# Optimization experiments

Measured on AMD Instinct MI355X. Metric: run time of the kernel, lower is better.

Reference implementation:

```python
import jax, jax.numpy as jnp
import numpy as np

BLUR_SIGMA = 5.0      # init kwarg blur_sigma
N_SIGMAS_PER_SIDE = 4 # fixed in module source
FLOW_AMP = 1.0        # init kwarg flow_amp
N_DIMS = 2            # len(img_shape) - 1


def _gaussian_kernel_2d(sigma, n_sigmas_per_side):
    # separable 2D gaussian spanning n_sigmas_per_side sigmas on each side, sum-normalized
    r = int(round(n_sigmas_per_side * sigma))
    x = np.arange(-r, r + 1, dtype=np.float32)
    g = np.exp(-(x ** 2) / (2.0 * sigma ** 2))
    k = np.outer(g, g)
    k /= k.sum()
    return jnp.asarray(k, dtype=jnp.float32)  # [kh, kw] = [41, 41] for sigma=5


def setup_inputs() -> dict:
    key = jax.random.key(0)
    k1, k2 = jax.random.split(key)
    inputs = jax.random.normal(k1, (16, 512, 512, 1), dtype=jnp.float32)
    # uniform in [0,1); scaled to [-flow_amp, flow_amp) inside reference
    rand_noise = jax.random.uniform(k2, (16, 512, 512, 2), dtype=jnp.float32)
    return {"inputs": inputs, "rand_noise": rand_noise}


def reference(inputs, rand_noise):
    # kernel tiled identically over the n_dims flow channels (depthwise, multiplier=1)
    k2d = _gaussian_kernel_2d(BLUR_SIGMA, N_SIGMAS_PER_SIDE)
    kernel = jnp.tile(k2d[:, :, None, None], (1, 1, 1, N_DIMS))  # HWIO: [41,41,1,2]
    # K.random_uniform(minval=-flow_amp, maxval=flow_amp)
    flow = rand_noise * (2.0 * FLOW_AMP) - FLOW_AMP  # [B,H,W,2]
    # tf.nn.depthwise_conv2d(..., strides=1, padding='SAME')
    out = jax.lax.conv_general_dilated(
        flow, kernel,
        window_strides=(1, 1),
        padding="SAME",
        dimension_numbers=("NHWC", "HWIO", "NHWC"),
        feature_group_count=N_DIMS,
    )  # [B,H,W,2] == reshape to (-1,)+flow_shape (no-op here)
    return out
```

## Files before the change

kernel.cpp:

```cpp
#include <hip/hip_runtime.h>

#define NB   16
#define H    512
#define W    512
#define KW   41
#define HALO 20

#define TX   88
#define TY   32
#define IN_W 128
#define PVV  16
#define PX   11
#define MSTR 129
#define OSTR 89
#define SMEM_F2 (TY * MSTR)

constexpr float G[KW] = {
  0.0003354626f, 0.0007318024f, 0.0015338104f, 0.0030887172f,
  0.0059760229f, 0.0111089965f, 0.0198410947f, 0.0340474548f,
  0.0561347628f, 0.0889216176f, 0.1353352832f, 0.1978986990f,
  0.2780373005f, 0.3753110988f, 0.4867522560f, 0.6065306597f,
  0.7261490371f, 0.8352702114f, 0.9231163464f, 0.9801986733f,
  1.0f,
  0.9801986733f, 0.9231163464f, 0.8352702114f, 0.7261490371f,
  0.6065306597f, 0.4867522560f, 0.3753110988f, 0.2780373005f,
  0.1978986990f, 0.1353352832f, 0.0889216176f, 0.0561347628f,
  0.0340474548f, 0.0198410947f, 0.0111089965f, 0.0059760229f,
  0.0030887172f, 0.0015338104f, 0.0007318024f, 0.0003354626f
};

constexpr float gsum() { float s = 0.f; for (int i = 0; i < KW; ++i) s += G[i]; return s; }
constexpr float INV_S2 = 1.0f / (gsum() * gsum());

__global__ __launch_bounds__(256, 4)
void randflow_blur_kernel(const float* __restrict__ noise, float* __restrict__ out) {
    __shared__ float2 smem[SMEM_F2];

    const int tid = threadIdx.x;
    const int bx  = blockIdx.x;
    const int tx0 = bx * TX;
    const int ty0 = blockIdx.y * TY;
    const int b   = blockIdx.z;
    const float* __restrict__ src = noise + (size_t)b * (H * W * 2);

    {
        const int sx  = tid & 127;
        const int yg  = tid >> 7;
        const int gx  = tx0 + sx - HALO;
        const int cgx = min(max(gx, 0), W - 1);
        const float sa = (gx == cgx) ? 2.0f : 0.0f;
        const float sb = (gx == cgx) ? -1.0f : 0.0f;
        const int  ysb = ty0 + yg * PVV - HALO;
        const float* __restrict__ colp = src + 2 * cgx;

        float2 acc[PVV];
        #pragma unroll
        for (int p = 0; p < PVV; ++p) acc[p] = make_float2(0.f, 0.f);

        #pragma unroll
        for (int j = 0; j < PVV + KW - 1; ++j) {
            const int ys = ysb + j;
            const int cy = min(max(ys, 0), H - 1);
            const float a  = (ys == cy) ? sa : 0.0f;
            const float bb = (ys == cy) ? sb : 0.0f;
            const float2 u = *(const float2*)(colp + (size_t)cy * (W * 2));
            float2 v;
            v.x = __builtin_fmaf(u.x, a, bb);
            v.y = __builtin_fmaf(u.y, a, bb);
            #pragma unroll
            for (int p = 0; p < PVV; ++p) {
                const int t = j - p;
                if (t >= 0 && t < KW) {
                    acc[p].x = __builtin_fmaf(G[t], v.x, acc[p].x);
                    acc[p].y = __builtin_fmaf(G[t], v.y, acc[p].y);
                }
            }
        }
        #pragma unroll
        for (int p = 0; p < PVV; ++p)
            smem[(yg * PVV + p) * MSTR + sx] = acc[p];
    }
    __syncthreads();

    const int y  = tid & 31;
    const int xg = tid >> 5;
    const int x0 = xg * PX;
    float2 facc[PX];
    {
        #pragma unroll
        for (int p = 0; p < PX; ++p) facc[p] = make_float2(0.f, 0.f);
        #pragma unroll
        for (int j = 0; j < PX + KW - 1; ++j) {
            const float2 v = smem[y * MSTR + x0 + j];
            #pragma unroll
            for (int p = 0; p < PX; ++p) {
                const int t = j - p;
                if (t >= 0 && t < KW) {
                    facc[p].x = __builtin_fmaf(G[t], v.x, facc[p].x);
                    facc[p].y = __builtin_fmaf(G[t], v.y, facc[p].y);
                }
            }
        }
    }
    __syncthreads();

    #pragma unroll
    for (int p = 0; p < PX; ++p) {
        float2 r;
        r.x = facc[p].x * INV_S2;
        r.y = facc[p].y * INV_S2;
        smem[y * OSTR + x0 + p] = r;
    }
    __syncthreads();

    #pragma unroll
    for (int p = 0; p < PX; ++p) {
        const int flat = p * 256 + tid;
        const int ry = flat / TX;
        const int rx = flat - ry * TX;
        const int xo = tx0 + rx;
        if (xo < W) {
            const int yo = ty0 + ry;
            *(float2*)(out + (((size_t)b * H + yo) * W + xo) * 2) = smem[ry * OSTR + rx];
        }
    }
}

extern "C" void kernel_launch(void* const* d_in, const int* in_sizes, int n_in,
                              void* d_out, int out_size, void* d_ws, size_t ws_size,
                              hipStream_t stream) {
    const float* noise = (const float*)d_in[1];
    float* out = (float*)d_out;

    dim3 grid((W + TX - 1) / TX, H / TY, NB);
    dim3 block(256);
    randflow_blur_kernel<<<grid, block, 0, stream>>>(noise, out);
}
```

Baseline: 124.6 us.

## Split fused blur into separate vertical and horizontal pass kernels via workspace

```diff
diff --git a/kernel.cpp b/kernel.cpp
--- a/kernel.cpp
+++ b/kernel.cpp
@@ -5,15 +5,6 @@
 #define W    512
 #define KW   41
 #define HALO 20
-
-#define TX   88
-#define TY   32
-#define IN_W 128
-#define PVV  16
-#define PX   11
-#define MSTR 129
-#define OSTR 89
-#define SMEM_F2 (TY * MSTR)
 
 constexpr float G[KW] = {
   0.0003354626f, 0.0007318024f, 0.0015338104f, 0.0030887172f,
@@ -31,6 +22,134 @@
 
 constexpr float gsum() { float s = 0.f; for (int i = 0; i < KW; ++i) s += G[i]; return s; }
 constexpr float INV_S2 = 1.0f / (gsum() * gsum());
+
+#define V_PV   16
+#define V_ROWS (V_PV + KW - 1)
+
+__global__ __launch_bounds__(256, 8)
+void vpass_kernel(const float* __restrict__ noise, float* __restrict__ mid) {
+    const int tid = threadIdx.x;
+
+    int id = blockIdx.x + 2 * (blockIdx.y + 32 * blockIdx.z);
+    id = ((id & 7) << 7) | (id >> 3);
+    const int lx = id & 1;
+    const int ly = (id >> 1) & 31;
+    const int lb = id >> 6;
+
+    const int x  = lx * 256 + tid;
+    const int y0 = ly * V_PV;
+
+    const float* __restrict__ src = noise + ((size_t)lb * H * W + x) * 2;
+    float*       __restrict__ dst = mid   + (((size_t)lb * H + y0) * W + x) * 2;
+
+    float2 acc[V_PV];
+    #pragma unroll
+    for (int p = 0; p < V_PV; ++p) acc[p] = make_float2(0.f, 0.f);
+
+    const int ysb = y0 - HALO;
+    #pragma unroll
+    for (int j = 0; j < V_ROWS; ++j) {
+        const int ys = ysb + j;
+        const int cy = min(max(ys, 0), H - 1);
+        const float a  = (ys == cy) ? 2.0f : 0.0f;
+        const float bb = (ys == cy) ? -1.0f : 0.0f;
+        const float2 u = *(const float2*)(src + (size_t)cy * (W * 2));
+        float2 v;
+        v.x = __builtin_fmaf(u.x, a, bb);
+        v.y = __builtin_fmaf(u.y, a, bb);
+        #pragma unroll
+        for (int p = 0; p < V_PV; ++p) {
+            const int t = j - p;
+            if (t >= 0 && t < KW) {
+                acc[p].x = __builtin_fmaf(G[t], v.x, acc[p].x);
+                acc[p].y = __builtin_fmaf(G[t], v.y, acc[p].y);
+            }
+        }
+    }
+    #pragma unroll
+    for (int p = 0; p < V_PV; ++p)
+        *(float2*)(dst + (size_t)p * (W * 2)) = acc[p];
+}
+
+#define HX   256
+#define HR   8
+#define HIN  (HX + 2 * HALO)
+#define HSTR 297
+#define HOSTR 257
+#define HPX  8
+
+__global__ __launch_bounds__(256, 8)
+void hpass_kernel(const float* __restrict__ mid, float* __restrict__ out) {
+    __shared__ float2 smem[HR * HSTR];
+
+    const int tid = threadIdx.x;
+    const int x0  = blockIdx.x * HX;
+    const int y0  = blockIdx.y * HR;
+    const int b   = blockIdx.z;
+
+    const float* __restrict__ srcb = mid + ((size_t)b * H + y0) * (W * 2);
+
+    #pragma unroll
+    for (int k = 0; k < 10; ++k) {
+        const int flat = tid + k * 256;
+        if (flat < HR * HIN) {
+            const int row = flat / HIN;
+            const int c   = flat - row * HIN;
+            const int gx  = x0 + c - HALO;
+            float2 v = make_float2(0.f, 0.f);
+            if ((unsigned)gx < W)
+                v = *(const float2*)(srcb + (size_t)row * (W * 2) + gx * 2);
+            smem[row * HSTR + c] = v;
+        }
+    }
+    __syncthreads();
+
+    const int y  = tid & 7;
+    const int xg = tid >> 3;
+    float2 facc[HPX];
+    #pragma unroll
+    for (int p = 0; p < HPX; ++p) facc[p] = make_float2(0.f, 0.f);
+    #pragma unroll
+    for (int j = 0; j < HPX + KW - 1; ++j) {
+        const float2 v = smem[y * HSTR + xg * HPX + j];
+        #pragma unroll
+        for (int p = 0; p < HPX; ++p) {
+            const int t = j - p;
+            if (t >= 0 && t < KW) {
+                facc[p].x = __builtin_fmaf(G[t], v.x, facc[p].x);
+                facc[p].y = __builtin_fmaf(G[t], v.y, facc[p].y);
+            }
+        }
+    }
+    __syncthreads();
+
+    #pragma unroll
+    for (int p = 0; p < HPX; ++p) {
+        float2 r;
+        r.x = facc[p].x * INV_S2;
+        r.y = facc[p].y * INV_S2;
+        smem[y * HOSTR + xg * HPX + p] = r;
+    }
+    __syncthreads();
+
+    float* __restrict__ ob = out + (((size_t)b * H + y0) * W + x0) * 2;
+    #pragma unroll
+    for (int k = 0; k < 8; ++k) {
+        const int flat = tid + k * 256;
+        const int row  = flat >> 8;
+        const int c    = flat & 255;
+        *(float2*)(ob + (size_t)row * (W * 2) + c * 2) = smem[row * HOSTR + c];
+    }
+}
+
+#define TX   88
+#define TY   32
+#define IN_W 128
+#define PVV  16
+#define PX   11
+#define MSTR 129
+#define OSTR 89
+#define SMEM_F2 (TY * MSTR)
 
 __global__ __launch_bounds__(256, 4)
 void randflow_blur_kernel(const float* __restrict__ noise, float* __restrict__ out) {
@@ -132,7 +251,13 @@
     const float* noise = (const float*)d_in[1];
     float* out = (float*)d_out;
 
-    dim3 grid((W + TX - 1) / TX, H / TY, NB);
-    dim3 block(256);
-    randflow_blur_kernel<<<grid, block, 0, stream>>>(noise, out);
-}
+    const size_t mid_bytes = (size_t)NB * H * W * 2 * sizeof(float);
+    if (d_ws != nullptr && ws_size >= mid_bytes) {
+        float* mid = (float*)d_ws;
+        vpass_kernel<<<dim3(2, 32, NB), dim3(256), 0, stream>>>(noise, mid);
+        hpass_kernel<<<dim3(2, H / HR, NB), dim3(256), 0, stream>>>(mid, out);
+    } else {
+        dim3 grid((W + TX - 1) / TX, H / TY, NB);
+        randflow_blur_kernel<<<grid, dim3(256), 0, stream>>>(noise, out);
+    }
+}
```

Result: slower. 218.8 us (+75.7%).

## Process full-width row strips per block to eliminate horizontal halo recompute

Applied to the files above, without the earlier changes.

```diff
diff --git a/kernel.cpp b/kernel.cpp
--- a/kernel.cpp
+++ b/kernel.cpp
@@ -6,14 +6,12 @@
 #define KW   41
 #define HALO 20
 
-#define TX   88
-#define TY   32
-#define IN_W 128
-#define PVV  16
-#define PX   11
-#define MSTR 129
-#define OSTR 89
-#define SMEM_F2 (TY * MSTR)
+#define FTY   16
+#define FROWS (FTY + KW - 1)
+#define PADW  (W + 2 * HALO)
+#define SSTR  553
+#define OSTR  513
+#define HPX   16
 
 constexpr float G[KW] = {
   0.0003354626f, 0.0007318024f, 0.0015338104f, 0.0030887172f,
@@ -32,43 +30,48 @@
 constexpr float gsum() { float s = 0.f; for (int i = 0; i < KW; ++i) s += G[i]; return s; }
 constexpr float INV_S2 = 1.0f / (gsum() * gsum());
 
-__global__ __launch_bounds__(256, 4)
-void randflow_blur_kernel(const float* __restrict__ noise, float* __restrict__ out) {
-    __shared__ float2 smem[SMEM_F2];
+__global__ __launch_bounds__(512, 4)
+void randflow_fused_kernel(const float* __restrict__ noise, float* __restrict__ out) {
+    __shared__ float2 smem[FTY * SSTR];
 
     const int tid = threadIdx.x;
-    const int bx  = blockIdx.x;
-    const int tx0 = bx * TX;
-    const int ty0 = blockIdx.y * TY;
-    const int b   = blockIdx.z;
-    const float* __restrict__ src = noise + (size_t)b * (H * W * 2);
+
+    int id = blockIdx.x + 32 * blockIdx.y;
+    id = ((id & 7) << 6) | (id >> 3);
+    const int ly = id & 31;
+    const int lb = id >> 5;
+    const int y0 = ly * FTY;
+
+    #pragma unroll
+    for (int k = 0; k < 2; ++k) {
+        const int flat = tid + k * 512;
+        if (flat < FTY * 2 * HALO) {
+            const int row = flat / 40;
+            const int c   = flat - row * 40;
+            const int col = (c < HALO) ? c : (c + W);
+            smem[row * SSTR + col] = make_float2(0.f, 0.f);
+        }
+    }
 
     {
-        const int sx  = tid & 127;
-        const int yg  = tid >> 7;
-        const int gx  = tx0 + sx - HALO;
-        const int cgx = min(max(gx, 0), W - 1);
-        const float sa = (gx == cgx) ? 2.0f : 0.0f;
-        const float sb = (gx == cgx) ? -1.0f : 0.0f;
-        const int  ysb = ty0 + yg * PVV - HALO;
-        const float* __restrict__ colp = src + 2 * cgx;
+        const float* __restrict__ src = noise + ((size_t)lb * H * W + tid) * 2;
+        float2 acc[FTY];
+        #pragma unroll
+        for (int p = 0; p < FTY; ++p) acc[p] = make_float2(0.f, 0.f);
 
-        float2 acc[PVV];
+        const int ysb = y0 - HALO;
         #pragma unroll
-        for (int p = 0; p < PVV; ++p) acc[p] = make_float2(0.f, 0.f);
-
-        #pragma unroll
-        for (int j = 0; j < PVV + KW - 1; ++j) {
+        for (int j = 0; j < FROWS; ++j) {
             const int ys = ysb + j;
             const int cy = min(max(ys, 0), H - 1);
-            const float a  = (ys == cy) ? sa : 0.0f;
-            const float bb = (ys == cy) ? sb : 0.0f;
-            const float2 u = *(const float2*)(colp + (size_t)cy * (W * 2));
+            const float a  = (ys == cy) ? 2.0f : 0.0f;
+            const float bb = (ys == cy) ? -1.0f : 0.0f;
+            const float2 u = *(const float2*)(src + (size_t)cy * (W * 2));
             float2 v;
             v.x = __builtin_fmaf(u.x, a, bb);
             v.y = __builtin_fmaf(u.y, a, bb);
             #pragma unroll
-            for (int p = 0; p < PVV; ++p) {
+            for (int p = 0; p < FTY; ++p) {
                 const int t = j - p;
                 if (t >= 0 && t < KW) {
                     acc[p].x = __builtin_fmaf(G[t], v.x, acc[p].x);
@@ -77,23 +80,23 @@
             }
         }
         #pragma unroll
-        for (int p = 0; p < PVV; ++p)
-            smem[(yg * PVV + p) * MSTR + sx] = acc[p];
+        for (int p = 0; p < FTY; ++p)
+            smem[p * SSTR + HALO + tid] = acc[p];
     }
     __syncthreads();
 
-    const int y  = tid & 31;
-    const int xg = tid >> 5;
-    const int x0 = xg * PX;
-    float2 facc[PX];
+    const int y  = tid & 15;
+    const int xg = tid >> 4;
+    const int x0 = xg * HPX;
+    float2 facc[HPX];
     {
         #pragma unroll
-        for (int p = 0; p < PX; ++p) facc[p] = make_float2(0.f, 0.f);
+        for (int p = 0; p < HPX; ++p) facc[p] = make_float2(0.f, 0.f);
         #pragma unroll
-        for (int j = 0; j < PX + KW - 1; ++j) {
-            const float2 v = smem[y * MSTR + x0 + j];
+        for (int j = 0; j < HPX + KW - 1; ++j) {
+            const float2 v = smem[y * SSTR + x0 + j];
             #pragma unroll
-            for (int p = 0; p < PX; ++p) {
+            for (int p = 0; p < HPX; ++p) {
                 const int t = j - p;
                 if (t >= 0 && t < KW) {
                     facc[p].x = __builtin_fmaf(G[t], v.x, facc[p].x);
@@ -105,7 +108,7 @@
     __syncthreads();
 
     #pragma unroll
-    for (int p = 0; p < PX; ++p) {
+    for (int p = 0; p < HPX; ++p) {
         float2 r;
         r.x = facc[p].x * INV_S2;
         r.y = facc[p].y * INV_S2;
@@ -113,17 +116,10 @@
     }
     __syncthreads();
 
+    float* __restrict__ ob = out + (((size_t)lb * H + y0) * W) * 2;
     #pragma unroll
-    for (int p = 0; p < PX; ++p) {
-        const int flat = p * 256 + tid;
-        const int ry = flat / TX;
-        const int rx = flat - ry * TX;
-        const int xo = tx0 + rx;
-        if (xo < W) {
-            const int yo = ty0 + ry;
-            *(float2*)(out + (((size_t)b * H + yo) * W + xo) * 2) = smem[ry * OSTR + rx];
-        }
-    }
+    for (int k = 0; k < FTY; ++k)
+        *(float2*)(ob + (size_t)k * (W * 2) + tid * 2) = smem[k * OSTR + tid];
 }
 
 extern "C" void kernel_launch(void* const* d_in, const int* in_sizes, int n_in,
@@ -132,7 +128,5 @@
     const float* noise = (const float*)d_in[1];
     float* out = (float*)d_out;
 
-    dim3 grid((W + TX - 1) / TX, H / TY, NB);
-    dim3 block(256);
-    randflow_blur_kernel<<<grid, block, 0, stream>>>(noise, out);
+    randflow_fused_kernel<<<dim3(H / FTY, NB), dim3(512), 0, stream>>>(noise, out);
 }
```

Result: faster. 108.5 us (-12.9%).
